# Kernel optimization log

Measured on AMD Instinct MI355X. Metric: run time of the kernel, lower is better.

The kernel has to match this reference:

```python
import jax, jax.numpy as jnp
import numpy as np


def setup_inputs() -> dict:
    key = jax.random.key(0)
    k1, k2 = jax.random.split(key)
    pred = jax.random.normal(k1, (8, 4096, 2), dtype=jnp.float32)
    target = jax.random.normal(k2, (8, 4096, 2), dtype=jnp.float32)
    return {"pred": pred, "target": target}


def reference(pred, target):
    # pred: [B, N, D], target: [B, M, D]
    # pairwise euclidean distances per batch: [B, N, M]
    diff = pred[:, :, None, :] - target[:, None, :, :]  # [B, N, M, D]
    dist = jnp.sqrt(jnp.sum(diff * diff, axis=-1))       # [B, N, M]
    # directed Hausdorff h(a,b) = max_i min_j d(a_i, b_j)
    h_ab = jnp.max(jnp.min(dist, axis=2), axis=1)        # [B]
    h_ba = jnp.max(jnp.min(dist, axis=1), axis=1)        # [B]
    score = jnp.maximum(h_ab, h_ba)                      # symmetric Hausdorff per batch
    return jnp.mean(score)
```

## Files before the change

### kernel.cpp

```cpp
#include <hip/hip_runtime.h>
#include <hip/hip_bf16.h>
#include <math.h>


#define B 8
#define N 4096
#define TPB 256
#define IB 8
#define JC 16
#define JTILE (N / JC)
#define ITILES (N / TPB)

__global__ __launch_bounds__(TPB) void hk_partial(const float* __restrict__ pred,
                                                  const float* __restrict__ target,
                                                  float* __restrict__ pw) {
    const int bx  = blockIdx.x;
    const int ib  = bx & 1;
    const int jc  = bx >> 1;
    const int b   = blockIdx.y;
    const int dir = blockIdx.z;

    const float2* __restrict__ P =
        reinterpret_cast<const float2*>(dir == 0 ? pred : target) + (size_t)b * N;
    const float*  __restrict__ Qf =
        (dir == 0 ? target : pred) + (size_t)b * N * 2 + (size_t)jc * JTILE * 2;

    __shared__ float4 sQ[JTILE / 2];
    if (threadIdx.x < JTILE / 2)
        sQ[threadIdx.x] = reinterpret_cast<const float4*>(Qf)[threadIdx.x];
    __syncthreads();

    float m2x[IB], m2y[IB], pp[IB], mn[IB];
    const int i0 = ib * (TPB * IB) + threadIdx.x;
    #pragma unroll
    for (int k = 0; k < IB; ++k) {
        float2 p = P[i0 + k * TPB];
        m2x[k] = -2.f * p.x;
        m2y[k] = -2.f * p.y;
        pp[k]  = fmaf(p.x, p.x, p.y * p.y);
        mn[k]  = 3.402823466e38f;
    }

    #pragma unroll 4
    for (int j = 0; j < JTILE / 2; ++j) {
        float4 q = sQ[j];
        float qqa = fmaf(q.x, q.x, q.y * q.y);
        float qqb = fmaf(q.z, q.z, q.w * q.w);
        #pragma unroll
        for (int k = 0; k < IB; ++k) {
            float ta = fmaf(m2x[k], q.x, fmaf(m2y[k], q.y, qqa));
            float tb = fmaf(m2x[k], q.z, fmaf(m2y[k], q.w, qqb));
            mn[k] = fminf(mn[k], fminf(ta, tb));
        }
    }

    float* dst = pw + (size_t)((dir * B + b) * JC + jc) * N;
    #pragma unroll
    for (int k = 0; k < IB; ++k)
        dst[i0 + k * TPB] = mn[k] + pp[k];
}

__global__ __launch_bounds__(TPB) void hk_maxred(const float* __restrict__ pw,
                                                 float* __restrict__ pw2) {
    const int tile = blockIdx.x;
    const int b    = blockIdx.y;
    const int dir  = blockIdx.z;
    const int t    = threadIdx.x;

    const float* base = pw + (size_t)((dir * B + b) * JC) * N + tile * TPB + t;
    float mnv = base[0];
    #pragma unroll
    for (int jc = 1; jc < JC; ++jc) mnv = fminf(mnv, base[(size_t)jc * N]);

    float mx = mnv;
    #pragma unroll
    for (int off = 32; off > 0; off >>= 1)
        mx = fmaxf(mx, __shfl_down(mx, off, 64));

    __shared__ float sred[TPB / 64];
    if ((t & 63) == 0) sred[t >> 6] = mx;
    __syncthreads();
    if (t == 0) {
        float bm = sred[0];
        #pragma unroll
        for (int w = 1; w < TPB / 64; ++w) bm = fmaxf(bm, sred[w]);
        pw2[(dir * B + b) * ITILES + tile] = bm;
    }
}

__global__ __launch_bounds__(64) void hk_final(const float* __restrict__ pw2,
                                               float* __restrict__ out) {
    const int t = threadIdx.x;
    __shared__ float h2[2 * B];
    if (t < 2 * B) {
        float mx = pw2[t * ITILES];
        #pragma unroll
        for (int k = 1; k < ITILES; ++k) mx = fmaxf(mx, pw2[t * ITILES + k]);
        h2[t] = mx;
    }
    __syncthreads();
    if (t == 0) {
        float s = 0.f;
        #pragma unroll
        for (int b = 0; b < B; ++b)
            s += sqrtf(fmaxf(fmaxf(h2[b], h2[B + b]), 0.f));
        out[0] = s * (1.0f / B);
    }
}

extern "C" void kernel_launch(void* const* d_in, const int* in_sizes, int n_in,
                              void* d_out, int out_size, void* d_ws, size_t ws_size,
                              hipStream_t stream) {
    const float* pred   = (const float*)d_in[0];
    const float* target = (const float*)d_in[1];
    float* out = (float*)d_out;
    float* pw  = (float*)d_ws;
    float* pw2 = (float*)((char*)d_ws + (size_t)2 * B * JC * N * sizeof(float));

    dim3 g1(32, B, 2);
    hk_partial<<<g1, TPB, 0, stream>>>(pred, target, pw);
    dim3 g2(ITILES, B, 2);
    hk_maxred<<<g2, TPB, 0, stream>>>(pw, pw2);
    hk_final<<<1, 64, 0, stream>>>(pw2, out);
}
```

Baseline: 78.63 us.

## Compute pairwise squared distances with split-fp16 MFMA instead of scalar FMAs

```diff
diff --git a/kernel.cpp b/kernel.cpp
--- a/kernel.cpp
+++ b/kernel.cpp
@@ -1,63 +1,100 @@
 #include <hip/hip_runtime.h>
-#include <hip/hip_bf16.h>
 #include <math.h>
 
 
 #define B 8
 #define N 4096
 #define TPB 256
-#define IB 8
-#define JC 16
+#define JC 8
 #define JTILE (N / JC)
+#define NT (JTILE / 32)
+#define IBLK 128
+#define NIB (N / IBLK)
 #define ITILES (N / TPB)
+
+typedef _Float16 half8 __attribute__((ext_vector_type(8)));
+typedef float f32x16 __attribute__((ext_vector_type(16)));
 
 __global__ __launch_bounds__(TPB) void hk_partial(const float* __restrict__ pred,
                                                   const float* __restrict__ target,
                                                   float* __restrict__ pw) {
-    const int bx  = blockIdx.x;
-    const int ib  = bx & 1;
-    const int jc  = bx >> 1;
+    const int ibk = blockIdx.x & (NIB - 1);
+    const int jc  = blockIdx.x >> 5;
     const int b   = blockIdx.y;
     const int dir = blockIdx.z;
 
     const float2* __restrict__ P =
         reinterpret_cast<const float2*>(dir == 0 ? pred : target) + (size_t)b * N;
-    const float*  __restrict__ Qf =
-        (dir == 0 ? target : pred) + (size_t)b * N * 2 + (size_t)jc * JTILE * 2;
+    const float2* __restrict__ Q =
+        reinterpret_cast<const float2*>(dir == 0 ? target : pred) + (size_t)b * N
+        + (size_t)jc * JTILE;
 
-    __shared__ float4 sQ[JTILE / 2];
-    if (threadIdx.x < JTILE / 2)
-        sQ[threadIdx.x] = reinterpret_cast<const float4*>(Qf)[threadIdx.x];
+    __shared__ half8 sA[NT * 64];
+
+    for (int s = threadIdx.x; s < JTILE; s += TPB) {
+        float2 q = Q[s];
+        _Float16 xh = (_Float16)q.x;
+        _Float16 xl = (_Float16)(q.x - (float)xh);
+        _Float16 yh = (_Float16)q.y;
+        _Float16 yl = (_Float16)(q.y - (float)yh);
+        float qq = fmaf(q.x, q.x, q.y * q.y);
+        _Float16 qqh = (_Float16)qq;
+        _Float16 qql = (_Float16)(qq - (float)qqh);
+        _Float16 nxh = (_Float16)(-2.f * (float)xh);
+        _Float16 nxl = (_Float16)(-2.f * (float)xl);
+        _Float16 nyh = (_Float16)(-2.f * (float)yh);
+        _Float16 nyl = (_Float16)(-2.f * (float)yl);
+        const _Float16 z = (_Float16)0.f;
+        int t = s >> 5, m = s & 31;
+        sA[t * 64 + m]      = (half8){nxh, nxh, nxl, nxl, nyh, nyh, nyl, nyl};
+        sA[t * 64 + 32 + m] = (half8){qqh, qql, z, z, z, z, z, z};
+    }
+
+    const int lane = threadIdx.x & 63;
+    const int wave = threadIdx.x >> 6;
+    const int col  = lane & 31;
+    const int i    = ibk * IBLK + wave * 32 + col;
+
+    half8 bf;
+    float pp = 0.f;
+    if (lane < 32) {
+        float2 p = P[i];
+        _Float16 xh = (_Float16)p.x;
+        _Float16 xl = (_Float16)(p.x - (float)xh);
+        _Float16 yh = (_Float16)p.y;
+        _Float16 yl = (_Float16)(p.y - (float)yh);
+        bf = (half8){xh, xl, xh, xl, yh, yl, yh, yl};
+        pp = fmaf(p.x, p.x, p.y * p.y);
+    } else {
+        const _Float16 one = (_Float16)1.f;
+        const _Float16 z   = (_Float16)0.f;
+        bf = (half8){one, one, z, z, z, z, z, z};
+    }
+
     __syncthreads();
 
-    float m2x[IB], m2y[IB], pp[IB], mn[IB];
-    const int i0 = ib * (TPB * IB) + threadIdx.x;
+    float rm[8];
     #pragma unroll
-    for (int k = 0; k < IB; ++k) {
-        float2 p = P[i0 + k * TPB];
-        m2x[k] = -2.f * p.x;
-        m2y[k] = -2.f * p.y;
-        pp[k]  = fmaf(p.x, p.x, p.y * p.y);
-        mn[k]  = 3.402823466e38f;
+    for (int r = 0; r < 8; ++r) rm[r] = 3.402823466e38f;
+
+    #pragma unroll 2
+    for (int t = 0; t < NT; ++t) {
+        half8 a = sA[t * 64 + lane];
+        f32x16 acc = {};
+        acc = __builtin_amdgcn_mfma_f32_32x32x16_f16(a, bf, acc, 0, 0, 0);
+        #pragma unroll
+        for (int r = 0; r < 8; ++r)
+            rm[r] = fminf(rm[r], fminf(acc[2 * r], acc[2 * r + 1]));
     }
 
-    #pragma unroll 4
-    for (int j = 0; j < JTILE / 2; ++j) {
-        float4 q = sQ[j];
-        float qqa = fmaf(q.x, q.x, q.y * q.y);
-        float qqb = fmaf(q.z, q.z, q.w * q.w);
-        #pragma unroll
-        for (int k = 0; k < IB; ++k) {
-            float ta = fmaf(m2x[k], q.x, fmaf(m2y[k], q.y, qqa));
-            float tb = fmaf(m2x[k], q.z, fmaf(m2y[k], q.w, qqb));
-            mn[k] = fminf(mn[k], fminf(ta, tb));
-        }
+    float mn = fminf(fminf(fminf(rm[0], rm[1]), fminf(rm[2], rm[3])),
+                     fminf(fminf(rm[4], rm[5]), fminf(rm[6], rm[7])));
+    mn = fminf(mn, __shfl_xor(mn, 32, 64));
+
+    if (lane < 32) {
+        float* dst = pw + (size_t)((dir * B + b) * JC + jc) * N;
+        dst[i] = mn + pp;
     }
-
-    float* dst = pw + (size_t)((dir * B + b) * JC + jc) * N;
-    #pragma unroll
-    for (int k = 0; k < IB; ++k)
-        dst[i0 + k * TPB] = mn[k] + pp[k];
 }
 
 __global__ __launch_bounds__(TPB) void hk_maxred(const float* __restrict__ pw,
@@ -117,7 +154,7 @@
     float* pw  = (float*)d_ws;
     float* pw2 = (float*)((char*)d_ws + (size_t)2 * B * JC * N * sizeof(float));
 
-    dim3 g1(32, B, 2);
+    dim3 g1(NIB * JC, B, 2);
     hk_partial<<<g1, TPB, 0, stream>>>(pred, target, pw);
     dim3 g2(ITILES, B, 2);
     hk_maxred<<<g2, TPB, 0, stream>>>(pw, pw2);
```

After: 79.28 us. No clear change (+0.8%).
